# Optimization experiments

Measured on AMD Instinct MI355X. Metric: run time of the kernel, lower is better.

Reference implementation:

```python
import jax, jax.numpy as jnp
import numpy as np

# Irrep layout of node_vec: 128x0e | 64x1e (64*3) | 32x2e (32*5)
MUL0, MUL1, MUL2 = 128, 64, 32
A = 32  # node_attr scalar channels (32x0e)
N = 8192


def setup_inputs() -> dict:
    key = jax.random.key(0)
    ks = jax.random.split(key, 12)
    f32 = jnp.float32
    return {
        "node_vec": jax.random.normal(ks[0], (N, MUL0 + 3 * MUL1 + 5 * MUL2), f32),
        "node_embedding": jax.random.normal(ks[1], (N, A), f32),
        # fctp_1: TP(input, attr) -> gated irreps (scalars + gates + vectors)
        "W1s": jax.random.normal(ks[2], (MUL0, A, MUL0), f32),          # 0e x 0e -> 0e
        "b1s": jnp.zeros((MUL0,), f32),
        "W1g": jax.random.normal(ks[3], (MUL0, A, MUL1 + MUL2), f32),   # 0e x 0e -> gate 0e
        "b1g": jnp.zeros((MUL1 + MUL2,), f32),
        "W1v1": jax.random.normal(ks[4], (MUL1, A, MUL1), f32),         # 1e x 0e -> 1e
        "W1v2": jax.random.normal(ks[5], (MUL2, A, MUL2), f32),         # 2e x 0e -> 2e
        # fctp_2: TP(mlp_mid, attr) -> 32x0e (only scalar path allowed by CG rules)
        "W2": jax.random.normal(ks[6], (MUL0, A, A), f32),
        "b2": jnp.zeros((A,), f32),
        # output network: LinearRS(32->32) + SiLU + LinearRS(32->1)
        "W3": jax.random.normal(ks[7], (A, A), f32),
        "b3": jnp.zeros((A,), f32),
        "W4": jax.random.normal(ks[8], (A, 1), f32),
        "b4": jnp.zeros((1,), f32),
    }


def reference(node_vec, node_embedding, W1s, b1s, W1g, b1g, W1v1, W1v2, W2, b2, W3, b3, W4, b4):
    n = node_vec.shape[0]
    attr = node_embedding
    # split features by irrep degree
    s = node_vec[:, :MUL0]                                         # [n,128]   0e
    v1 = node_vec[:, MUL0:MUL0 + 3 * MUL1].reshape(n, MUL1, 3)     # [n,64,3]  1e
    v2 = node_vec[:, MUL0 + 3 * MUL1:].reshape(n, MUL2, 5)         # [n,32,5]  2e

    inv = lambda u: 1.0 / np.sqrt(u * A).astype(np.float32)

    # ---- fctp_1: fully-connected TP with scalar attr (l x 0e -> l per-path mixing) ----
    s_mid = jnp.einsum('nu,nv,uvw->nw', s, attr, W1s) * inv(MUL0) + b1s
    g = jnp.einsum('nu,nv,uvw->nw', s, attr, W1g) * inv(MUL0) + b1g
    v1_mid = jnp.einsum('num,nv,uvw->nwm', v1, attr, W1v1) * inv(MUL1)
    v2_mid = jnp.einsum('num,nv,uvw->nwm', v2, attr, W1v2) * inv(MUL2)

    # ---- SwishGate: SiLU on scalars, sigmoid gates on vectors ----
    s_act = jax.nn.silu(s_mid)
    gate = jax.nn.sigmoid(g)
    v1_g = v1_mid * gate[:, :MUL1, None]
    v2_g = v2_mid * gate[:, MUL1:, None]
    # NOTE: v1_g/v2_g have no allowed CG path into the 0e output of fctp_2 (l x 0 -> 0
    # only for l=0), so they do not contribute — exactly as in the original module.
    del v1_g, v2_g

    # ---- fctp_2: mlp_mid x attr -> 32x0e (scalar path only) ----
    h = jnp.einsum('nu,nv,uvw->nw', s_act, attr, W2) * inv(MUL0) + b2

    # ---- output network: LinearRS + SiLU + LinearRS ----
    h = jax.nn.silu(h @ (W3 / np.sqrt(A).astype(np.float32)) + b3)
    pred_energy = h @ (W4 / np.sqrt(A).astype(np.float32)) + b4     # [n,1]
    return pred_energy
```

## Files before the change

kernel.cpp:

```cpp
#include <hip/hip_runtime.h>

typedef _Float16 f16;
typedef f16 f16x8 __attribute__((ext_vector_type(8)));
typedef f16 f16x4 __attribute__((ext_vector_type(4)));
typedef f16 f16x2 __attribute__((ext_vector_type(2)));
typedef float f32x4 __attribute__((ext_vector_type(4)));

__global__ __launch_bounds__(256) void prep_kernel(
    const float* __restrict__ node_vec, const float* __restrict__ attr,
    const float* __restrict__ W1s, const float* __restrict__ W2,
    f16* __restrict__ s_f16, f16* __restrict__ attr_f16,
    f16* __restrict__ W1P, f16* __restrict__ W2P)
{
    __shared__ f16 T[32 * 36];
    const int b = blockIdx.x, t = threadIdx.x;

    if (b < 640) {
        const float* src; f16* dst; int u, w0, W;
        if (b < 512) { u = b >> 2; w0 = (b & 3) * 32; W = 128; src = W1s; dst = W1P; }
        else         { u = b - 512; w0 = 0;           W = 32;  src = W2;  dst = W2P; }
        {
            int v = t >> 3, wq = t & 7;
            float4 f = *(const float4*)(src + (size_t)(u * 32 + v) * W + w0 + wq * 4);
            T[v * 36 + wq * 4 + 0] = (f16)f.x;
            T[v * 36 + wq * 4 + 1] = (f16)f.y;
            T[v * 36 + wq * 4 + 2] = (f16)f.z;
            T[v * 36 + wq * 4 + 3] = (f16)f.w;
        }
        __syncthreads();
        {
            int w = t >> 3, vr = t & 7;
            f16x4 o = { T[(vr * 4 + 0) * 36 + w], T[(vr * 4 + 1) * 36 + w],
                        T[(vr * 4 + 2) * 36 + w], T[(vr * 4 + 3) * 36 + w] };
            *(f16x4*)(dst + (size_t)u * (W * 32) + (size_t)(w0 + w) * 32 + vr * 4) = o;
        }
    } else if (b < 1152) {
        int j = (b - 640) * 256 + t;
        int n = j >> 4, c = j & 15;
        float4 a  = *(const float4*)(node_vec + (size_t)n * 480 + c * 8);
        float4 bb = *(const float4*)(node_vec + (size_t)n * 480 + c * 8 + 4);
        f16x8 ev = { (f16)a.x, (f16)a.y, (f16)a.z, (f16)a.w,
                     (f16)bb.x, (f16)bb.y, (f16)bb.z, (f16)bb.w };
        *(f16x8*)(s_f16 + (size_t)n * 128 + c * 8) = ev;
    } else {
        int j = (b - 1152) * 256 + t;
        int n = j >> 2, c = j & 3;
        float4 a  = *(const float4*)(attr + (size_t)n * 32 + c * 8);
        float4 bb = *(const float4*)(attr + (size_t)n * 32 + c * 8 + 4);
        f16x8 ev = { (f16)a.x, (f16)a.y, (f16)a.z, (f16)a.w,
                     (f16)bb.x, (f16)bb.y, (f16)bb.z, (f16)bb.w };
        *(f16x8*)(attr_f16 + (size_t)n * 32 + c * 8) = ev;
    }
}

__global__ __launch_bounds__(512) void fused_kernel(
    const f16* __restrict__ s_f16, const f16* __restrict__ attr_f16,
    const f16* __restrict__ W1P, const f16* __restrict__ W2P,
    const float* __restrict__ b1s, const float* __restrict__ b2,
    const float* __restrict__ W3, const float* __restrict__ b3,
    const float* __restrict__ W4, const float* __restrict__ b4,
    float* __restrict__ out)
{
    __shared__ alignas(16) f16 s_lds[32 * 136];
    __shared__ alignas(16) f16 sact_lds[32 * 136];
    __shared__ alignas(16) float W3_lds[32 * 36];
    __shared__ alignas(16) float h_lds[2][32 * 36];

    const int t = threadIdx.x;
    const int n0 = blockIdx.x * 32;
    const int wv = t >> 6, l = t & 63, lr = l & 15, q = l >> 4;

    { int r = t >> 4, pt = t & 15;
      *(uint4*)(s_lds + r * 136 + pt * 8) =
          *(const uint4*)(s_f16 + (size_t)(n0 + r) * 128 + pt * 8); }
    if (t < 256) { int i = t >> 3, j = (t & 7) * 4;
      *(f32x4*)(W3_lds + i * 36 + j) = *(const f32x4*)(W3 + i * 32 + j); }

    f16x2 attrh[2][4];
    #pragma unroll
    for (int mt = 0; mt < 2; ++mt)
        #pragma unroll
        for (int kk = 0; kk < 4; ++kk)
            attrh[mt][kk] = *(const f16x2*)(attr_f16 +
                (size_t)(n0 + 16 * mt + lr) * 32 + q * 8 + kk * 2);

    __syncthreads();

    const f16* Bbase = W1P + (16 * wv + lr) * 32 + q * 8;
    f16x8 bfrag[4];
    #pragma unroll
    for (int i = 0; i < 4; ++i) bfrag[i] = *(const f16x8*)(Bbase + i * 4096);
    f16 sv[2][2];
    #pragma unroll
    for (int pp = 0; pp < 2; ++pp) {
        sv[pp][0] = s_lds[lr * 136 + pp];
        sv[pp][1] = s_lds[(16 + lr) * 136 + pp];
    }

    f32x4 acc0 = {0.f, 0.f, 0.f, 0.f}, acc1 = {0.f, 0.f, 0.f, 0.f};
    #pragma unroll 4
    for (int c = 0; c < 128; ++c) {
        f16x8 bf = bfrag[c & 3];
        int cn = (c + 4 < 128) ? c + 4 : 127;
        bfrag[c & 3] = *(const f16x8*)(Bbase + (size_t)cn * 4096);
        f16 s0 = sv[c & 1][0], s1 = sv[c & 1][1];
        int cs = (c + 2 < 128) ? c + 2 : 127;
        sv[c & 1][0] = s_lds[lr * 136 + cs];
        sv[c & 1][1] = s_lds[(16 + lr) * 136 + cs];
        f16x2 s02 = {s0, s0}, s12 = {s1, s1};
        f16x8 a0, a1;
        #pragma unroll
        for (int kk = 0; kk < 4; ++kk) {
            f16x2 p0 = s02 * attrh[0][kk];
            f16x2 p1 = s12 * attrh[1][kk];
            a0[2 * kk] = p0[0]; a0[2 * kk + 1] = p0[1];
            a1[2 * kk] = p1[0]; a1[2 * kk + 1] = p1[1];
        }
        acc0 = __builtin_amdgcn_mfma_f32_16x16x32_f16(a0, bf, acc0, 0, 0, 0);
        acc1 = __builtin_amdgcn_mfma_f32_16x16x32_f16(a1, bf, acc1, 0, 0, 0);
    }

    {
        float b1v = b1s[16 * wv + lr];
        #pragma unroll
        for (int reg = 0; reg < 4; ++reg) {
            float v0 = acc0[reg] * 0.015625f + b1v;
            float v1 = acc1[reg] * 0.015625f + b1v;
            float g0 = v0 / (1.f + __expf(-v0));
            float g1 = v1 / (1.f + __expf(-v1));
            sact_lds[(q * 4 + reg) * 136 + 16 * wv + lr] = (f16)g0;
            sact_lds[(16 + q * 4 + reg) * 136 + 16 * wv + lr] = (f16)g1;
        }
    }
    __syncthreads();

    const int wm = wv & 1, wn = (wv >> 1) & 1, kh = wv >> 2;
    f16x2 aw[4];
    #pragma unroll
    for (int kk = 0; kk < 4; ++kk) aw[kk] = wm ? attrh[1][kk] : attrh[0][kk];

    const f16* B2base = W2P + (size_t)kh * 64 * 1024 + (16 * wn + lr) * 32 + q * 8;
    const int srow = (16 * wm + lr) * 136 + kh * 64;
    f16x8 b2frag[4];
    #pragma unroll
    for (int i = 0; i < 4; ++i) b2frag[i] = *(const f16x8*)(B2base + i * 1024);
    f16 sv2[2];
    sv2[0] = sact_lds[srow + 0];
    sv2[1] = sact_lds[srow + 1];

    f32x4 acc2 = {0.f, 0.f, 0.f, 0.f};
    #pragma unroll 4
    for (int cc = 0; cc < 64; ++cc) {
        f16x8 bf = b2frag[cc & 3];
        int cn = (cc + 4 < 64) ? cc + 4 : 63;
        b2frag[cc & 3] = *(const f16x8*)(B2base + (size_t)cn * 1024);
        f16 s0 = sv2[cc & 1];
        int cs = (cc + 2 < 64) ? cc + 2 : 63;
        sv2[cc & 1] = sact_lds[srow + cs];
        f16x2 ss = {s0, s0};
        f16x8 a0;
        #pragma unroll
        for (int kk = 0; kk < 4; ++kk) {
            f16x2 p = ss * aw[kk];
            a0[2 * kk] = p[0]; a0[2 * kk + 1] = p[1];
        }
        acc2 = __builtin_amdgcn_mfma_f32_16x16x32_f16(a0, bf, acc2, 0, 0, 0);
    }
    {
        float b2v = (kh == 0) ? b2[16 * wn + lr] : 0.f;
        #pragma unroll
        for (int reg = 0; reg < 4; ++reg)
            h_lds[kh][(16 * wm + q * 4 + reg) * 36 + 16 * wn + lr] =
                acc2[reg] * 0.015625f + b2v;
    }
    __syncthreads();

    {
        int hn = t >> 4, j0 = (t & 15) * 2;
        float a0 = 0.f, a1 = 0.f;
        #pragma unroll
        for (int i = 0; i < 32; ++i) {
            float hv = h_lds[0][hn * 36 + i] + h_lds[1][hn * 36 + i];
            a0 += hv * W3_lds[i * 36 + j0];
            a1 += hv * W3_lds[i * 36 + j0 + 1];
        }
        const float inv = 0.17677669529663687f;
        float t0 = a0 * inv + b3[j0];
        float t1 = a1 * inv + b3[j0 + 1];
        float g0 = t0 / (1.f + __expf(-t0));
        float g1 = t1 / (1.f + __expf(-t1));
        float p = g0 * W4[j0] * inv + g1 * W4[j0 + 1] * inv;
        p += __shfl_xor(p, 1);
        p += __shfl_xor(p, 2);
        p += __shfl_xor(p, 4);
        p += __shfl_xor(p, 8);
        if ((t & 15) == 0) out[n0 + hn] = p + b4[0];
    }
}

extern "C" void kernel_launch(void* const* d_in, const int* in_sizes, int n_in,
                              void* d_out, int out_size, void* d_ws, size_t ws_size,
                              hipStream_t stream)
{
    const float* node_vec = (const float*)d_in[0];
    const float* attr     = (const float*)d_in[1];
    const float* W1s      = (const float*)d_in[2];
    const float* b1s      = (const float*)d_in[3];
    const float* W2       = (const float*)d_in[8];
    const float* b2       = (const float*)d_in[9];
    const float* W3       = (const float*)d_in[10];
    const float* b3       = (const float*)d_in[11];
    const float* W4       = (const float*)d_in[12];
    const float* b4       = (const float*)d_in[13];
    float* out = (float*)d_out;

    char* ws = (char*)d_ws;
    f16* s_f16    = (f16*)(ws);
    f16* attr_f16 = (f16*)(ws + (2u << 20));
    f16* W1P      = (f16*)(ws + (2560u << 10));
    f16* W2P      = (f16*)(ws + (3584u << 10));

    prep_kernel<<<1280, 256, 0, stream>>>(node_vec, attr, W1s, W2,
                                          s_f16, attr_f16, W1P, W2P);
    fused_kernel<<<256, 512, 0, stream>>>(s_f16, attr_f16, W1P, W2P,
                                          b1s, b2, W3, b3, W4, b4, out);
}
```

Before: 117.3 us.

## Fuse activation fp16 conversion into main kernel and retile both MFMA stages

The prep kernel no longer converts node_vec scalars and attr to fp16. The fused kernel now reads the fp32 inputs directly and converts them on load, which removes a global write and re-read of the intermediates. The first GEMM is retiled so each wave owns one row half and 32 output columns: s rows are held in registers and B fragments are double-buffered in groups of 4. This cuts the per-step LDS loads of s but raises register pressure. The second GEMM splits K four ways and computes both row tiles per wave, which needs four partial h buffers in LDS that are summed in the epilogue.

```diff
diff --git a/kernel.cpp b/kernel.cpp
--- a/kernel.cpp
+++ b/kernel.cpp
@@ -7,56 +7,36 @@
 typedef float f32x4 __attribute__((ext_vector_type(4)));
 
 __global__ __launch_bounds__(256) void prep_kernel(
-    const float* __restrict__ node_vec, const float* __restrict__ attr,
     const float* __restrict__ W1s, const float* __restrict__ W2,
-    f16* __restrict__ s_f16, f16* __restrict__ attr_f16,
     f16* __restrict__ W1P, f16* __restrict__ W2P)
 {
     __shared__ f16 T[32 * 36];
     const int b = blockIdx.x, t = threadIdx.x;
 
-    if (b < 640) {
-        const float* src; f16* dst; int u, w0, W;
-        if (b < 512) { u = b >> 2; w0 = (b & 3) * 32; W = 128; src = W1s; dst = W1P; }
-        else         { u = b - 512; w0 = 0;           W = 32;  src = W2;  dst = W2P; }
-        {
-            int v = t >> 3, wq = t & 7;
-            float4 f = *(const float4*)(src + (size_t)(u * 32 + v) * W + w0 + wq * 4);
-            T[v * 36 + wq * 4 + 0] = (f16)f.x;
-            T[v * 36 + wq * 4 + 1] = (f16)f.y;
-            T[v * 36 + wq * 4 + 2] = (f16)f.z;
-            T[v * 36 + wq * 4 + 3] = (f16)f.w;
-        }
-        __syncthreads();
-        {
-            int w = t >> 3, vr = t & 7;
-            f16x4 o = { T[(vr * 4 + 0) * 36 + w], T[(vr * 4 + 1) * 36 + w],
-                        T[(vr * 4 + 2) * 36 + w], T[(vr * 4 + 3) * 36 + w] };
-            *(f16x4*)(dst + (size_t)u * (W * 32) + (size_t)(w0 + w) * 32 + vr * 4) = o;
-        }
-    } else if (b < 1152) {
-        int j = (b - 640) * 256 + t;
-        int n = j >> 4, c = j & 15;
-        float4 a  = *(const float4*)(node_vec + (size_t)n * 480 + c * 8);
-        float4 bb = *(const float4*)(node_vec + (size_t)n * 480 + c * 8 + 4);
-        f16x8 ev = { (f16)a.x, (f16)a.y, (f16)a.z, (f16)a.w,
-                     (f16)bb.x, (f16)bb.y, (f16)bb.z, (f16)bb.w };
-        *(f16x8*)(s_f16 + (size_t)n * 128 + c * 8) = ev;
-    } else {
-        int j = (b - 1152) * 256 + t;
-        int n = j >> 2, c = j & 3;
-        float4 a  = *(const float4*)(attr + (size_t)n * 32 + c * 8);
-        float4 bb = *(const float4*)(attr + (size_t)n * 32 + c * 8 + 4);
-        f16x8 ev = { (f16)a.x, (f16)a.y, (f16)a.z, (f16)a.w,
-                     (f16)bb.x, (f16)bb.y, (f16)bb.z, (f16)bb.w };
-        *(f16x8*)(attr_f16 + (size_t)n * 32 + c * 8) = ev;
+    const float* src; f16* dst; int u, w0, W;
+    if (b < 512) { u = b >> 2; w0 = (b & 3) * 32; W = 128; src = W1s; dst = W1P; }
+    else         { u = b - 512; w0 = 0;           W = 32;  src = W2;  dst = W2P; }
+    {
+        int v = t >> 3, wq = t & 7;
+        float4 f = *(const float4*)(src + (size_t)(u * 32 + v) * W + w0 + wq * 4);
+        T[v * 36 + wq * 4 + 0] = (f16)f.x;
+        T[v * 36 + wq * 4 + 1] = (f16)f.y;
+        T[v * 36 + wq * 4 + 2] = (f16)f.z;
+        T[v * 36 + wq * 4 + 3] = (f16)f.w;
+    }
+    __syncthreads();
+    {
+        int w = t >> 3, vr = t & 7;
+        f16x4 o = { T[(vr * 4 + 0) * 36 + w], T[(vr * 4 + 1) * 36 + w],
+                    T[(vr * 4 + 2) * 36 + w], T[(vr * 4 + 3) * 36 + w] };
+        *(f16x4*)(dst + (size_t)u * (W * 32) + (size_t)(w0 + w) * 32 + vr * 4) = o;
     }
 }
 
 __global__ __launch_bounds__(512) void fused_kernel(
-    const f16* __restrict__ s_f16, const f16* __restrict__ attr_f16,
+    const float* __restrict__ node_vec, const float* __restrict__ attr,
     const f16* __restrict__ W1P, const f16* __restrict__ W2P,
-    const float* __restrict__ b1s, const float* __restrict__ b2,
+    const float* __restrict__ b1s, const float* __restrict__ bias2,
     const float* __restrict__ W3, const float* __restrict__ b3,
     const float* __restrict__ W4, const float* __restrict__ b4,
     float* __restrict__ out)
@@ -64,114 +44,144 @@
     __shared__ alignas(16) f16 s_lds[32 * 136];
     __shared__ alignas(16) f16 sact_lds[32 * 136];
     __shared__ alignas(16) float W3_lds[32 * 36];
-    __shared__ alignas(16) float h_lds[2][32 * 36];
-
-    const int t = threadIdx.x;
+    __shared__ alignas(16) float h_lds[4][32 * 36];
+
+    const int t  = threadIdx.x;
     const int n0 = blockIdx.x * 32;
     const int wv = t >> 6, l = t & 63, lr = l & 15, q = l >> 4;
 
-    { int r = t >> 4, pt = t & 15;
-      *(uint4*)(s_lds + r * 136 + pt * 8) =
-          *(const uint4*)(s_f16 + (size_t)(n0 + r) * 128 + pt * 8); }
-    if (t < 256) { int i = t >> 3, j = (t & 7) * 4;
-      *(f32x4*)(W3_lds + i * 36 + j) = *(const f32x4*)(W3 + i * 32 + j); }
+    #pragma unroll
+    for (int i = 0; i < 2; ++i) {
+        int idx = t + 512 * i;
+        int r = idx >> 5, c4 = idx & 31;
+        float4 f = *(const float4*)(node_vec + (size_t)(n0 + r) * 480 + c4 * 4);
+        f16x4 o = { (f16)f.x, (f16)f.y, (f16)f.z, (f16)f.w };
+        *(f16x4*)(s_lds + r * 136 + c4 * 4) = o;
+    }
+    if (t < 256) {
+        int i = t >> 3, j = (t & 7) * 4;
+        *(f32x4*)(W3_lds + i * 36 + j) = *(const f32x4*)(W3 + i * 32 + j);
+    }
 
     f16x2 attrh[2][4];
     #pragma unroll
     for (int mt = 0; mt < 2; ++mt)
         #pragma unroll
-        for (int kk = 0; kk < 4; ++kk)
-            attrh[mt][kk] = *(const f16x2*)(attr_f16 +
-                (size_t)(n0 + 16 * mt + lr) * 32 + q * 8 + kk * 2);
-
-    __syncthreads();
-
-    const f16* Bbase = W1P + (16 * wv + lr) * 32 + q * 8;
-    f16x8 bfrag[4];
-    #pragma unroll
-    for (int i = 0; i < 4; ++i) bfrag[i] = *(const f16x8*)(Bbase + i * 4096);
-    f16 sv[2][2];
-    #pragma unroll
-    for (int pp = 0; pp < 2; ++pp) {
-        sv[pp][0] = s_lds[lr * 136 + pp];
-        sv[pp][1] = s_lds[(16 + lr) * 136 + pp];
+        for (int kk = 0; kk < 4; ++kk) {
+            float2 f = *(const float2*)(attr + (size_t)(n0 + 16 * mt + lr) * 32 + q * 8 + kk * 2);
+            attrh[mt][kk] = f16x2{ (f16)f.x, (f16)f.y };
+        }
+
+    __syncthreads();
+
+    const int wm = wv & 1, cg = wv >> 1;
+
+    f16x8 s8[16];
+    {
+        const f16* srow = s_lds + (16 * wm + lr) * 136;
+        #pragma unroll
+        for (int ch = 0; ch < 16; ++ch) s8[ch] = *(const f16x8*)(srow + ch * 8);
+    }
+
+    const f16* B0 = W1P + (32 * cg + lr) * 32 + q * 8;
+    const f16* B1 = B0 + 16 * 32;
+
+    f16x8 bb[2][2][4];
+    #pragma unroll
+    for (int j = 0; j < 4; ++j) {
+        bb[0][0][j] = *(const f16x8*)(B0 + (size_t)j * 4096);
+        bb[0][1][j] = *(const f16x8*)(B1 + (size_t)j * 4096);
     }
 
     f32x4 acc0 = {0.f, 0.f, 0.f, 0.f}, acc1 = {0.f, 0.f, 0.f, 0.f};
-    #pragma unroll 4
-    for (int c = 0; c < 128; ++c) {
-        f16x8 bf = bfrag[c & 3];
-        int cn = (c + 4 < 128) ? c + 4 : 127;
-        bfrag[c & 3] = *(const f16x8*)(Bbase + (size_t)cn * 4096);
-        f16 s0 = sv[c & 1][0], s1 = sv[c & 1][1];
-        int cs = (c + 2 < 128) ? c + 2 : 127;
-        sv[c & 1][0] = s_lds[lr * 136 + cs];
-        sv[c & 1][1] = s_lds[(16 + lr) * 136 + cs];
-        f16x2 s02 = {s0, s0}, s12 = {s1, s1};
-        f16x8 a0, a1;
-        #pragma unroll
-        for (int kk = 0; kk < 4; ++kk) {
-            f16x2 p0 = s02 * attrh[0][kk];
-            f16x2 p1 = s12 * attrh[1][kk];
-            a0[2 * kk] = p0[0]; a0[2 * kk + 1] = p0[1];
-            a1[2 * kk] = p1[0]; a1[2 * kk + 1] = p1[1];
-        }
-        acc0 = __builtin_amdgcn_mfma_f32_16x16x32_f16(a0, bf, acc0, 0, 0, 0);
-        acc1 = __builtin_amdgcn_mfma_f32_16x16x32_f16(a1, bf, acc1, 0, 0, 0);
-    }
-
-    {
-        float b1v = b1s[16 * wv + lr];
+    #pragma unroll
+    for (int g = 0; g < 32; ++g) {
+        const int buf = g & 1, nbuf = buf ^ 1;
+        const int gn = (g + 1 < 32) ? g + 1 : 31;
+        #pragma unroll
+        for (int j = 0; j < 4; ++j) {
+            bb[nbuf][0][j] = *(const f16x8*)(B0 + (size_t)(4 * gn + j) * 4096);
+            bb[nbuf][1][j] = *(const f16x8*)(B1 + (size_t)(4 * gn + j) * 4096);
+        }
+        #pragma unroll
+        for (int j = 0; j < 4; ++j) {
+            const int c = 4 * g + j;
+            f16 sv = s8[c >> 3][c & 7];
+            f16x2 sb = { sv, sv };
+            f16x8 a;
+            #pragma unroll
+            for (int kk = 0; kk < 4; ++kk) {
+                f16x2 p = sb * attrh[wm][kk];
+                a[2 * kk] = p[0]; a[2 * kk + 1] = p[1];
+            }
+            acc0 = __builtin_amdgcn_mfma_f32_16x16x32_f16(a, bb[buf][0][j], acc0, 0, 0, 0);
+            acc1 = __builtin_amdgcn_mfma_f32_16x16x32_f16(a, bb[buf][1][j], acc1, 0, 0, 0);
+        }
+    }
+
+    {
+        float bv0 = b1s[32 * cg + lr];
+        float bv1 = b1s[32 * cg + 16 + lr];
         #pragma unroll
         for (int reg = 0; reg < 4; ++reg) {
-            float v0 = acc0[reg] * 0.015625f + b1v;
-            float v1 = acc1[reg] * 0.015625f + b1v;
-            float g0 = v0 / (1.f + __expf(-v0));
-            float g1 = v1 / (1.f + __expf(-v1));
-            sact_lds[(q * 4 + reg) * 136 + 16 * wv + lr] = (f16)g0;
-            sact_lds[(16 + q * 4 + reg) * 136 + 16 * wv + lr] = (f16)g1;
-        }
-    }
-    __syncthreads();
-
-    const int wm = wv & 1, wn = (wv >> 1) & 1, kh = wv >> 2;
-    f16x2 aw[4];
-    #pragma unroll
-    for (int kk = 0; kk < 4; ++kk) aw[kk] = wm ? attrh[1][kk] : attrh[0][kk];
-
-    const f16* B2base = W2P + (size_t)kh * 64 * 1024 + (16 * wn + lr) * 32 + q * 8;
-    const int srow = (16 * wm + lr) * 136 + kh * 64;
-    f16x8 b2frag[4];
-    #pragma unroll
-    for (int i = 0; i < 4; ++i) b2frag[i] = *(const f16x8*)(B2base + i * 1024);
-    f16 sv2[2];
-    sv2[0] = sact_lds[srow + 0];
-    sv2[1] = sact_lds[srow + 1];
-
-    f32x4 acc2 = {0.f, 0.f, 0.f, 0.f};
-    #pragma unroll 4
-    for (int cc = 0; cc < 64; ++cc) {
-        f16x8 bf = b2frag[cc & 3];
-        int cn = (cc + 4 < 64) ? cc + 4 : 63;
-        b2frag[cc & 3] = *(const f16x8*)(B2base + (size_t)cn * 1024);
-        f16 s0 = sv2[cc & 1];
-        int cs = (cc + 2 < 64) ? cc + 2 : 63;
-        sv2[cc & 1] = sact_lds[srow + cs];
-        f16x2 ss = {s0, s0};
-        f16x8 a0;
-        #pragma unroll
-        for (int kk = 0; kk < 4; ++kk) {
-            f16x2 p = ss * aw[kk];
-            a0[2 * kk] = p[0]; a0[2 * kk + 1] = p[1];
-        }
-        acc2 = __builtin_amdgcn_mfma_f32_16x16x32_f16(a0, bf, acc2, 0, 0, 0);
-    }
-    {
-        float b2v = (kh == 0) ? b2[16 * wn + lr] : 0.f;
-        #pragma unroll
-        for (int reg = 0; reg < 4; ++reg)
-            h_lds[kh][(16 * wm + q * 4 + reg) * 36 + 16 * wn + lr] =
-                acc2[reg] * 0.015625f + b2v;
+            int row = 16 * wm + q * 4 + reg;
+            float v0 = acc0[reg] * 0.015625f + bv0;
+            float v1 = acc1[reg] * 0.015625f + bv1;
+            sact_lds[row * 136 + 32 * cg + lr]      = (f16)(v0 / (1.f + __expf(-v0)));
+            sact_lds[row * 136 + 32 * cg + 16 + lr] = (f16)(v1 / (1.f + __expf(-v1)));
+        }
+    }
+    __syncthreads();
+
+    const int wn = wv & 1, kq = wv >> 1;
+
+    f16x8 sa[2][4];
+    #pragma unroll
+    for (int mt = 0; mt < 2; ++mt) {
+        const f16* srow = sact_lds + (16 * mt + lr) * 136 + kq * 32;
+        #pragma unroll
+        for (int ch = 0; ch < 4; ++ch) sa[mt][ch] = *(const f16x8*)(srow + ch * 8);
+    }
+
+    const f16* B2 = W2P + (size_t)(kq * 32) * 1024 + (16 * wn + lr) * 32 + q * 8;
+
+    f16x8 b2b[2][4];
+    #pragma unroll
+    for (int j = 0; j < 4; ++j) b2b[0][j] = *(const f16x8*)(B2 + (size_t)j * 1024);
+
+    f32x4 acc20 = {0.f, 0.f, 0.f, 0.f}, acc21 = {0.f, 0.f, 0.f, 0.f};
+    #pragma unroll
+    for (int g = 0; g < 8; ++g) {
+        const int buf = g & 1, nbuf = buf ^ 1;
+        const int gn = (g + 1 < 8) ? g + 1 : 7;
+        #pragma unroll
+        for (int j = 0; j < 4; ++j)
+            b2b[nbuf][j] = *(const f16x8*)(B2 + (size_t)(4 * gn + j) * 1024);
+        #pragma unroll
+        for (int j = 0; j < 4; ++j) {
+            const int c = 4 * g + j;
+            f16 sv0 = sa[0][c >> 3][c & 7];
+            f16 sv1 = sa[1][c >> 3][c & 7];
+            f16x2 sb0 = { sv0, sv0 }, sb1 = { sv1, sv1 };
+            f16x8 a0, a1;
+            #pragma unroll
+            for (int kk = 0; kk < 4; ++kk) {
+                f16x2 p0 = sb0 * attrh[0][kk];
+                f16x2 p1 = sb1 * attrh[1][kk];
+                a0[2 * kk] = p0[0]; a0[2 * kk + 1] = p0[1];
+                a1[2 * kk] = p1[0]; a1[2 * kk + 1] = p1[1];
+            }
+            acc20 = __builtin_amdgcn_mfma_f32_16x16x32_f16(a0, b2b[buf][j], acc20, 0, 0, 0);
+            acc21 = __builtin_amdgcn_mfma_f32_16x16x32_f16(a1, b2b[buf][j], acc21, 0, 0, 0);
+        }
+    }
+    {
+        float bv = (kq == 0) ? bias2[16 * wn + lr] : 0.f;
+        #pragma unroll
+        for (int reg = 0; reg < 4; ++reg) {
+            h_lds[kq][(q * 4 + reg) * 36 + 16 * wn + lr]        = acc20[reg] * 0.015625f + bv;
+            h_lds[kq][(16 + q * 4 + reg) * 36 + 16 * wn + lr]   = acc21[reg] * 0.015625f + bv;
+        }
     }
     __syncthreads();
 
@@ -180,7 +190,8 @@
         float a0 = 0.f, a1 = 0.f;
         #pragma unroll
         for (int i = 0; i < 32; ++i) {
-            float hv = h_lds[0][hn * 36 + i] + h_lds[1][hn * 36 + i];
+            float hv = h_lds[0][hn * 36 + i] + h_lds[1][hn * 36 + i]
+                     + h_lds[2][hn * 36 + i] + h_lds[3][hn * 36 + i];
             a0 += hv * W3_lds[i * 36 + j0];
             a1 += hv * W3_lds[i * 36 + j0 + 1];
         }
@@ -215,13 +226,10 @@
     float* out = (float*)d_out;
 
     char* ws = (char*)d_ws;
-    f16* s_f16    = (f16*)(ws);
-    f16* attr_f16 = (f16*)(ws + (2u << 20));
-    f16* W1P      = (f16*)(ws + (2560u << 10));
-    f16* W2P      = (f16*)(ws + (3584u << 10));
-
-    prep_kernel<<<1280, 256, 0, stream>>>(node_vec, attr, W1s, W2,
-                                          s_f16, attr_f16, W1P, W2P);
-    fused_kernel<<<256, 512, 0, stream>>>(s_f16, attr_f16, W1P, W2P,
+    f16* W1P = (f16*)(ws);
+    f16* W2P = (f16*)(ws + (1u << 20));
+
+    prep_kernel<<<640, 256, 0, stream>>>(W1s, W2, W1P, W2P);
+    fused_kernel<<<256, 512, 0, stream>>>(node_vec, attr, W1P, W2P,
                                           b1s, b2, W3, b3, W4, b4, out);
 }
```

Measured after the change: 156.1 us. 1.33x slower.

## Split fused kernel into register-tiled GEMM1 and GEMM2+head kernels

Applied to the files above, without the earlier changes.

Replaces the single fused kernel with two kernels. The first computes the first tensor-product GEMM over 64-node tiles, splits output columns across a 2D grid and keeps four M-tiles per wave so each W1 fragment feeds four MFMAs. It writes the SiLU activations to a workspace buffer in f16. The second kernel runs the W2 GEMM with a K-split across waves and an LDS reduction, then the output MLP head. The aim is more reuse of weight loads and more MFMA work per load, at the cost of an extra launch and a global round-trip for the intermediate activations.

```diff
diff --git a/kernel.cpp b/kernel.cpp
--- a/kernel.cpp
+++ b/kernel.cpp
@@ -5,6 +5,8 @@
 typedef f16 f16x4 __attribute__((ext_vector_type(4)));
 typedef f16 f16x2 __attribute__((ext_vector_type(2)));
 typedef float f32x4 __attribute__((ext_vector_type(4)));
+
+union F8 { uint4 u4; f16x8 v; f16x2 h[4]; f16 e[8]; };
 
 __global__ __launch_bounds__(256) void prep_kernel(
     const float* __restrict__ node_vec, const float* __restrict__ attr,
@@ -53,148 +55,203 @@
     }
 }
 
-__global__ __launch_bounds__(512) void fused_kernel(
+__global__ __launch_bounds__(256, 2) void gemm1_kernel(
     const f16* __restrict__ s_f16, const f16* __restrict__ attr_f16,
-    const f16* __restrict__ W1P, const f16* __restrict__ W2P,
-    const float* __restrict__ b1s, const float* __restrict__ b2,
+    const f16* __restrict__ W1P, const float* __restrict__ b1s,
+    f16* __restrict__ s_act)
+{
+    __shared__ alignas(16) f16 s_lds[64 * 136];
+
+    const int t  = threadIdx.x;
+    const int n0 = blockIdx.x * 64;
+    const int l  = t & 63, lr = l & 15, q = l >> 4;
+    const int c0 = blockIdx.y * 64 + (t >> 6) * 16;
+
+    const f16* Bp = W1P + ((size_t)(c0 + lr)) * 32 + q * 8;
+    f16x8 B[8];
+    #pragma unroll
+    for (int j = 0; j < 8; ++j)
+        B[j] = *(const f16x8*)(Bp + (size_t)j * 4096);
+
+    F8 af[4];
+    #pragma unroll
+    for (int mt = 0; mt < 4; ++mt)
+        af[mt].v = *(const f16x8*)(attr_f16 + (size_t)(n0 + 16 * mt + lr) * 32 + q * 8);
+
+    #pragma unroll
+    for (int i = 0; i < 4; ++i) {
+        int ch = t + 256 * i;
+        int r = ch >> 4, c8 = ch & 15;
+        *(uint4*)(s_lds + r * 136 + c8 * 8) =
+            *(const uint4*)(s_f16 + (size_t)(n0 + r) * 128 + c8 * 8);
+    }
+    __syncthreads();
+
+    f32x4 acc[4] = { {0,0,0,0}, {0,0,0,0}, {0,0,0,0}, {0,0,0,0} };
+
+    F8 s8[2][4];
+    #pragma unroll
+    for (int mt = 0; mt < 4; ++mt)
+        s8[0][mt].v = *(const f16x8*)(s_lds + (16 * mt + lr) * 136);
+
+    #pragma unroll 4
+    for (int uo = 0; uo < 16; ++uo) {
+        const int cur = uo & 1, nxt = cur ^ 1;
+        const int uon = (uo + 1 < 16) ? uo + 1 : 15;
+        #pragma unroll
+        for (int mt = 0; mt < 4; ++mt)
+            s8[nxt][mt].v = *(const f16x8*)(s_lds + (16 * mt + lr) * 136 + uon * 8);
+        #pragma unroll
+        for (int j = 0; j < 8; ++j) {
+            const int u = uo * 8 + j;
+            f16x8 bf = B[j];
+            const int un = (u + 8 < 128) ? (u + 8) : u;
+            B[j] = *(const f16x8*)(Bp + (size_t)un * 4096);
+            #pragma unroll
+            for (int mt = 0; mt < 4; ++mt) {
+                f16 sv = s8[cur][mt].e[j];
+                f16x2 sb = { sv, sv };
+                F8 a;
+                #pragma unroll
+                for (int kk = 0; kk < 4; ++kk)
+                    a.h[kk] = sb * af[mt].h[kk];
+                acc[mt] = __builtin_amdgcn_mfma_f32_16x16x32_f16(a.v, bf, acc[mt], 0, 0, 0);
+            }
+        }
+    }
+
+    const float bv = b1s[c0 + lr];
+    #pragma unroll
+    for (int mt = 0; mt < 4; ++mt)
+        #pragma unroll
+        for (int reg = 0; reg < 4; ++reg) {
+            int row = n0 + 16 * mt + q * 4 + reg;
+            float v = acc[mt][reg] * 0.015625f + bv;
+            s_act[(size_t)row * 128 + c0 + lr] = (f16)(v / (1.f + __expf(-v)));
+        }
+}
+
+__global__ __launch_bounds__(256, 2) void gemm2_head_kernel(
+    const f16* __restrict__ s_act, const f16* __restrict__ attr_f16,
+    const f16* __restrict__ W2P, const float* __restrict__ b2,
     const float* __restrict__ W3, const float* __restrict__ b3,
     const float* __restrict__ W4, const float* __restrict__ b4,
     float* __restrict__ out)
 {
     __shared__ alignas(16) f16 s_lds[32 * 136];
-    __shared__ alignas(16) f16 sact_lds[32 * 136];
+    __shared__ alignas(16) float red[4][32 * 36];
     __shared__ alignas(16) float W3_lds[32 * 36];
-    __shared__ alignas(16) float h_lds[2][32 * 36];
-
-    const int t = threadIdx.x;
+    __shared__ alignas(16) float h_lds[32 * 36];
+
+    const int t  = threadIdx.x;
     const int n0 = blockIdx.x * 32;
     const int wv = t >> 6, l = t & 63, lr = l & 15, q = l >> 4;
-
-    { int r = t >> 4, pt = t & 15;
-      *(uint4*)(s_lds + r * 136 + pt * 8) =
-          *(const uint4*)(s_f16 + (size_t)(n0 + r) * 128 + pt * 8); }
-    if (t < 256) { int i = t >> 3, j = (t & 7) * 4;
-      *(f32x4*)(W3_lds + i * 36 + j) = *(const f32x4*)(W3 + i * 32 + j); }
-
-    f16x2 attrh[2][4];
+    const int u0 = wv * 32;
+
+    const f16* B2p = W2P + ((size_t)u0 * 32 + lr) * 32 + q * 8;
+    f16x8 B0[8], B1[8];
+    #pragma unroll
+    for (int j = 0; j < 8; ++j) {
+        B0[j] = *(const f16x8*)(B2p + (size_t)j * 1024);
+        B1[j] = *(const f16x8*)(B2p + (size_t)j * 1024 + 512);
+    }
+
+    F8 af[2];
     #pragma unroll
     for (int mt = 0; mt < 2; ++mt)
-        #pragma unroll
-        for (int kk = 0; kk < 4; ++kk)
-            attrh[mt][kk] = *(const f16x2*)(attr_f16 +
-                (size_t)(n0 + 16 * mt + lr) * 32 + q * 8 + kk * 2);
-
-    __syncthreads();
-
-    const f16* Bbase = W1P + (16 * wv + lr) * 32 + q * 8;
-    f16x8 bfrag[4];
-    #pragma unroll
-    for (int i = 0; i < 4; ++i) bfrag[i] = *(const f16x8*)(Bbase + i * 4096);
-    f16 sv[2][2];
-    #pragma unroll
-    for (int pp = 0; pp < 2; ++pp) {
-        sv[pp][0] = s_lds[lr * 136 + pp];
-        sv[pp][1] = s_lds[(16 + lr) * 136 + pp];
-    }
-
-    f32x4 acc0 = {0.f, 0.f, 0.f, 0.f}, acc1 = {0.f, 0.f, 0.f, 0.f};
-    #pragma unroll 4
-    for (int c = 0; c < 128; ++c) {
-        f16x8 bf = bfrag[c & 3];
-        int cn = (c + 4 < 128) ? c + 4 : 127;
-        bfrag[c & 3] = *(const f16x8*)(Bbase + (size_t)cn * 4096);
-        f16 s0 = sv[c & 1][0], s1 = sv[c & 1][1];
-        int cs = (c + 2 < 128) ? c + 2 : 127;
-        sv[c & 1][0] = s_lds[lr * 136 + cs];
-        sv[c & 1][1] = s_lds[(16 + lr) * 136 + cs];
-        f16x2 s02 = {s0, s0}, s12 = {s1, s1};
-        f16x8 a0, a1;
-        #pragma unroll
-        for (int kk = 0; kk < 4; ++kk) {
-            f16x2 p0 = s02 * attrh[0][kk];
-            f16x2 p1 = s12 * attrh[1][kk];
-            a0[2 * kk] = p0[0]; a0[2 * kk + 1] = p0[1];
-            a1[2 * kk] = p1[0]; a1[2 * kk + 1] = p1[1];
-        }
-        acc0 = __builtin_amdgcn_mfma_f32_16x16x32_f16(a0, bf, acc0, 0, 0, 0);
-        acc1 = __builtin_amdgcn_mfma_f32_16x16x32_f16(a1, bf, acc1, 0, 0, 0);
-    }
+        af[mt].v = *(const f16x8*)(attr_f16 + (size_t)(n0 + 16 * mt + lr) * 32 + q * 8);
+
+    #pragma unroll
+    for (int i = 0; i < 2; ++i) {
+        int ch = t + 256 * i;
+        int r = ch >> 4, c8 = ch & 15;
+        *(uint4*)(s_lds + r * 136 + c8 * 8) =
+            *(const uint4*)(s_act + (size_t)(n0 + r) * 128 + c8 * 8);
+    }
+    { int i = t >> 3, jj = (t & 7) * 4;
+      *(f32x4*)(W3_lds + i * 36 + jj) = *(const f32x4*)(W3 + i * 32 + jj); }
+    __syncthreads();
+
+    f32x4 acc[2][2] = { { {0,0,0,0}, {0,0,0,0} }, { {0,0,0,0}, {0,0,0,0} } };
+
+    F8 s8[2][2];
+    #pragma unroll
+    for (int mt = 0; mt < 2; ++mt)
+        s8[0][mt].v = *(const f16x8*)(s_lds + (16 * mt + lr) * 136 + u0);
+
+    #pragma unroll
+    for (int uo = 0; uo < 4; ++uo) {
+        const int cur = uo & 1, nxt = cur ^ 1;
+        const int uon = (uo + 1 < 4) ? uo + 1 : 3;
+        #pragma unroll
+        for (int mt = 0; mt < 2; ++mt)
+            s8[nxt][mt].v = *(const f16x8*)(s_lds + (16 * mt + lr) * 136 + u0 + uon * 8);
+        #pragma unroll
+        for (int j = 0; j < 8; ++j) {
+            const int k = uo * 8 + j;
+            f16x8 bf0 = B0[j], bf1 = B1[j];
+            const int kn = (k + 8 < 32) ? (k + 8) : k;
+            B0[j] = *(const f16x8*)(B2p + (size_t)kn * 1024);
+            B1[j] = *(const f16x8*)(B2p + (size_t)kn * 1024 + 512);
+            #pragma unroll
+            for (int mt = 0; mt < 2; ++mt) {
+                f16 sv = s8[cur][mt].e[j];
+                f16x2 sb = { sv, sv };
+                F8 a;
+                #pragma unroll
+                for (int kk = 0; kk < 4; ++kk)
+                    a.h[kk] = sb * af[mt].h[kk];
+                acc[mt][0] = __builtin_amdgcn_mfma_f32_16x16x32_f16(a.v, bf0, acc[mt][0], 0, 0, 0);
+                acc[mt][1] = __builtin_amdgcn_mfma_f32_16x16x32_f16(a.v, bf1, acc[mt][1], 0, 0, 0);
+            }
+        }
+    }
+
+    #pragma unroll
+    for (int mt = 0; mt < 2; ++mt)
+        #pragma unroll
+        for (int nt = 0; nt < 2; ++nt)
+            #pragma unroll
+            for (int reg = 0; reg < 4; ++reg)
+                red[wv][(16 * mt + q * 4 + reg) * 36 + 16 * nt + lr] = acc[mt][nt][reg];
+    __syncthreads();
 
     {
-        float b1v = b1s[16 * wv + lr];
-        #pragma unroll
-        for (int reg = 0; reg < 4; ++reg) {
-            float v0 = acc0[reg] * 0.015625f + b1v;
-            float v1 = acc1[reg] * 0.015625f + b1v;
-            float g0 = v0 / (1.f + __expf(-v0));
-            float g1 = v1 / (1.f + __expf(-v1));
-            sact_lds[(q * 4 + reg) * 136 + 16 * wv + lr] = (f16)g0;
-            sact_lds[(16 + q * 4 + reg) * 136 + 16 * wv + lr] = (f16)g1;
-        }
-    }
-    __syncthreads();
-
-    const int wm = wv & 1, wn = (wv >> 1) & 1, kh = wv >> 2;
-    f16x2 aw[4];
-    #pragma unroll
-    for (int kk = 0; kk < 4; ++kk) aw[kk] = wm ? attrh[1][kk] : attrh[0][kk];
-
-    const f16* B2base = W2P + (size_t)kh * 64 * 1024 + (16 * wn + lr) * 32 + q * 8;
-    const int srow = (16 * wm + lr) * 136 + kh * 64;
-    f16x8 b2frag[4];
-    #pragma unroll
-    for (int i = 0; i < 4; ++i) b2frag[i] = *(const f16x8*)(B2base + i * 1024);
-    f16 sv2[2];
-    sv2[0] = sact_lds[srow + 0];
-    sv2[1] = sact_lds[srow + 1];
-
-    f32x4 acc2 = {0.f, 0.f, 0.f, 0.f};
-    #pragma unroll 4
-    for (int cc = 0; cc < 64; ++cc) {
-        f16x8 bf = b2frag[cc & 3];
-        int cn = (cc + 4 < 64) ? cc + 4 : 63;
-        b2frag[cc & 3] = *(const f16x8*)(B2base + (size_t)cn * 1024);
-        f16 s0 = sv2[cc & 1];
-        int cs = (cc + 2 < 64) ? cc + 2 : 63;
-        sv2[cc & 1] = sact_lds[srow + cs];
-        f16x2 ss = {s0, s0};
-        f16x8 a0;
-        #pragma unroll
-        for (int kk = 0; kk < 4; ++kk) {
-            f16x2 p = ss * aw[kk];
-            a0[2 * kk] = p[0]; a0[2 * kk + 1] = p[1];
-        }
-        acc2 = __builtin_amdgcn_mfma_f32_16x16x32_f16(a0, bf, acc2, 0, 0, 0);
-    }
+        int row = t >> 3, c4 = (t & 7) * 4;
+        f32x4 s = *(const f32x4*)(&red[0][row * 36 + c4]);
+        s = s + *(const f32x4*)(&red[1][row * 36 + c4]);
+        s = s + *(const f32x4*)(&red[2][row * 36 + c4]);
+        s = s + *(const f32x4*)(&red[3][row * 36 + c4]);
+        #pragma unroll
+        for (int e = 0; e < 4; ++e)
+            h_lds[row * 36 + c4 + e] = s[e] * 0.015625f + b2[c4 + e];
+    }
+    __syncthreads();
+
     {
-        float b2v = (kh == 0) ? b2[16 * wn + lr] : 0.f;
-        #pragma unroll
-        for (int reg = 0; reg < 4; ++reg)
-            h_lds[kh][(16 * wm + q * 4 + reg) * 36 + 16 * wn + lr] =
-                acc2[reg] * 0.015625f + b2v;
-    }
-    __syncthreads();
-
-    {
-        int hn = t >> 4, j0 = (t & 15) * 2;
-        float a0 = 0.f, a1 = 0.f;
+        int node = t >> 3, j4 = (t & 7) * 4;
+        float a0 = 0.f, a1 = 0.f, a2 = 0.f, a3 = 0.f;
         #pragma unroll
         for (int i = 0; i < 32; ++i) {
-            float hv = h_lds[0][hn * 36 + i] + h_lds[1][hn * 36 + i];
-            a0 += hv * W3_lds[i * 36 + j0];
-            a1 += hv * W3_lds[i * 36 + j0 + 1];
+            float hv = h_lds[node * 36 + i];
+            a0 += hv * W3_lds[i * 36 + j4 + 0];
+            a1 += hv * W3_lds[i * 36 + j4 + 1];
+            a2 += hv * W3_lds[i * 36 + j4 + 2];
+            a3 += hv * W3_lds[i * 36 + j4 + 3];
         }
         const float inv = 0.17677669529663687f;
-        float t0 = a0 * inv + b3[j0];
-        float t1 = a1 * inv + b3[j0 + 1];
-        float g0 = t0 / (1.f + __expf(-t0));
-        float g1 = t1 / (1.f + __expf(-t1));
-        float p = g0 * W4[j0] * inv + g1 * W4[j0 + 1] * inv;
+        float p = 0.f;
+        float aa[4] = { a0, a1, a2, a3 };
+        #pragma unroll
+        for (int e = 0; e < 4; ++e) {
+            float tv = aa[e] * inv + b3[j4 + e];
+            float g  = tv / (1.f + __expf(-tv));
+            p += g * W4[j4 + e] * inv;
+        }
         p += __shfl_xor(p, 1);
         p += __shfl_xor(p, 2);
         p += __shfl_xor(p, 4);
-        p += __shfl_xor(p, 8);
-        if ((t & 15) == 0) out[n0 + hn] = p + b4[0];
+        if ((t & 7) == 0) out[n0 + node] = p + b4[0];
     }
 }
 
@@ -216,12 +273,14 @@
 
     char* ws = (char*)d_ws;
     f16* s_f16    = (f16*)(ws);
-    f16* attr_f16 = (f16*)(ws + (2u << 20));
+    f16* attr_f16 = (f16*)(ws + (2u   << 20));
     f16* W1P      = (f16*)(ws + (2560u << 10));
     f16* W2P      = (f16*)(ws + (3584u << 10));
+    f16* s_act    = (f16*)(ws + (3840u << 10));
 
     prep_kernel<<<1280, 256, 0, stream>>>(node_vec, attr, W1s, W2,
                                           s_f16, attr_f16, W1P, W2P);
-    fused_kernel<<<256, 512, 0, stream>>>(s_f16, attr_f16, W1P, W2P,
-                                          b1s, b2, W3, b3, W4, b4, out);
-}
+    gemm1_kernel<<<dim3(128, 2), 256, 0, stream>>>(s_f16, attr_f16, W1P, b1s, s_act);
+    gemm2_head_kernel<<<256, 256, 0, stream>>>(s_act, attr_f16, W2P, b2,
+                                               W3, b3, W4, b4, out);
+}
```

New measurement: 121.4 us. 1.03x slower.
